# Optimization experiments

Measured on AMD Instinct MI355X. Metric: run time of the kernel, lower is better.

The kernel has to match this reference:

```python
import jax, jax.numpy as jnp
import numpy as np

POOL_SCALES = (1, 3, 6, 8)
CHANNELS = 256
BN_EPS = 1e-5


def _pool_matrix(in_size, out_size):
    # Row i averages input slots [floor(i*in/out), ceil((i+1)*in/out)) -- matches AdaptiveAvgPool2d.
    P = np.zeros((out_size, in_size), np.float32)
    for i in range(out_size):
        s = (i * in_size) // out_size
        e = -((-(i + 1) * in_size) // out_size)
        P[i, s:e] = 1.0 / (e - s)
    return jnp.asarray(P)


def _bn(x, g, b, m, v):
    # inference-mode BatchNorm2d on NCHW
    inv = g * jax.lax.rsqrt(v + BN_EPS)
    return x * inv[None, :, None, None] + (b - m * inv)[None, :, None, None]


def _conv1x1(x, w):
    # 1x1 conv == channel matmul: w [Cout, Cin], x [B, Cin, H, W]
    return jnp.einsum('oc,bchw->bohw', w, x)


def _ppm_concat(x):
    # x: [B, C, H, W] -> [B, C, sum(s*s)]
    B, C, H, W = x.shape
    outs = []
    for s in POOL_SCALES:
        Ph = _pool_matrix(H, s)
        Pw = _pool_matrix(W, s)
        pooled = jnp.einsum('ih,jw,bchw->bcij', Ph, Pw, x)
        outs.append(pooled.reshape(B, C, -1))
    return jnp.concatenate(outs, axis=2)


def setup_inputs() -> dict:
    key = jax.random.key(0)
    ks = jax.random.split(key, 24)
    B, Cl, Ch, Cmid, Cout, H, W = 8, 1024, 2048, 256, 2048, 64, 64
    return {
        'low_feats': jax.random.normal(ks[0], (B, Cl, H, W), jnp.float32),
        'high_feats': jax.random.normal(ks[1], (B, Ch, H, W), jnp.float32),
        'q_w': jax.random.normal(ks[2], (Cmid, Ch), jnp.float32) * 0.02,
        'q_g': jax.random.uniform(ks[3], (Cmid,), jnp.float32, 0.5, 1.5),
        'q_b': jax.random.normal(ks[4], (Cmid,), jnp.float32) * 0.1,
        'q_m': jax.random.normal(ks[5], (Cmid,), jnp.float32) * 0.1,
        'q_v': jax.random.uniform(ks[6], (Cmid,), jnp.float32, 0.5, 1.5),
        'k_w': jax.random.normal(ks[7], (Cmid, Cl), jnp.float32) * 0.02,
        'k_g': jax.random.uniform(ks[8], (Cmid,), jnp.float32, 0.5, 1.5),
        'k_b': jax.random.normal(ks[9], (Cmid,), jnp.float32) * 0.1,
        'k_m': jax.random.normal(ks[10], (Cmid,), jnp.float32) * 0.1,
        'k_v': jax.random.uniform(ks[11], (Cmid,), jnp.float32, 0.5, 1.5),
        'v_w': jax.random.normal(ks[12], (Cmid, Cl), jnp.float32) * 0.02,
        'v_b': jax.random.normal(ks[13], (Cmid,), jnp.float32) * 0.02,
        'o_w': jax.random.normal(ks[14], (Cout, Cmid), jnp.float32) * 0.02,
        'o_b': jax.random.normal(ks[15], (Cout,), jnp.float32) * 0.02,
        'bn_w': jax.random.normal(ks[16], (Cout, Cout + Ch), jnp.float32) * 0.02,
        'bn_g': jax.random.uniform(ks[17], (Cout,), jnp.float32, 0.5, 1.5),
        'bn_b': jax.random.normal(ks[18], (Cout,), jnp.float32) * 0.1,
        'bn_m': jax.random.normal(ks[19], (Cout,), jnp.float32) * 0.1,
        'bn_v': jax.random.uniform(ks[20], (Cout,), jnp.float32, 0.5, 1.5),
    }


def reference(low_feats, high_feats, q_w, q_g, q_b, q_m, q_v,
              k_w, k_g, k_b, k_m, k_v, v_w, v_b, o_w, o_b,
              bn_w, bn_g, bn_b, bn_m, bn_v):
    B, _, H, W = high_feats.shape
    # query: ConvModule (1x1 conv, BN, ReLU) on high-level feats; query_scale=1 -> no downsample
    q = jax.nn.relu(_bn(_conv1x1(high_feats, q_w), q_g, q_b, q_m, q_v))
    q = q.reshape(B, CHANNELS, H * W).transpose(0, 2, 1)  # [B, N, C]
    # key: ConvModule then pyramid-pooled; value: plain 1x1 conv then pyramid-pooled
    k = jax.nn.relu(_bn(_conv1x1(low_feats, k_w), k_g, k_b, k_m, k_v))
    k = _ppm_concat(k)  # [B, C, M]
    v = _conv1x1(low_feats, v_w) + v_b[None, :, None, None]
    v = _ppm_concat(v).transpose(0, 2, 1)  # [B, M, C]
    # matmul-normalized attention with pooled K/V (M = 110, tiny)
    sim = jnp.einsum('bnc,bcm->bnm', q, k) * (CHANNELS ** -0.5)
    sim = jax.nn.softmax(sim, axis=-1)
    ctx = jnp.einsum('bnm,bmc->bnc', sim, v)  # [B, N, C]
    ctx = ctx.transpose(0, 2, 1).reshape(B, CHANNELS, H, W)
    # out projection: plain 1x1 conv with bias
    ctx = _conv1x1(ctx, o_w) + o_b[None, :, None, None]  # [B, Cout, H, W]
    # single stage (query_scales=(1,)), stack+sum is identity
    # bottleneck: 1x1 conv (no bias) + BN, no activation
    fused = jnp.concatenate([ctx, high_feats], axis=1)
    out = _bn(_conv1x1(fused, bn_w), bn_g, bn_b, bn_m, bn_v)
    return out
```

## Files before the change

### kernel.cpp

```cpp
#include <hip/hip_runtime.h>
#include <hip/hip_bf16.h>

typedef unsigned int u32;
typedef unsigned short u16;
typedef short s16x8 __attribute__((ext_vector_type(8)));
typedef float f32x4 __attribute__((ext_vector_type(4)));
typedef u16 u16x4 __attribute__((ext_vector_type(4)));

__device__ __forceinline__ u16 f2b(float x) {
  u32 u = __float_as_uint(x);
  return (u16)((u + 0x7fffu + ((u >> 16) & 1u)) >> 16);
}
__device__ __forceinline__ float b2f(u16 x) { return __uint_as_float(((u32)x) << 16); }

__device__ __forceinline__ void gload16(const void* g, void* l) {
  __builtin_amdgcn_global_load_lds((const __attribute__((address_space(1))) u32*)g,
                                   (__attribute__((address_space(3))) u32*)l, 16, 0, 0);
}
__device__ __forceinline__ f32x4 mfma16(s16x8 a, s16x8 b, f32x4 c) {
  return __builtin_amdgcn_mfma_f32_16x16x32_bf16(a, b, c, 0, 0, 0);
}

template <int OUT_BF16>
__global__ __launch_bounds__(512, 2) void gemm256(
    const u16* __restrict__ A, long long sA, int lda,
    const u16* __restrict__ B1, long long sB1, int K1,
    const u16* __restrict__ B2, long long sB2, int K2,
    void* __restrict__ Cv, long long sC, int ldc,
    const float* __restrict__ bias, int bias_mode,
    int relu_limit, float alpha) {
  const int K = K1 + K2, nt = K >> 6;
  int tm, tn, b;
  {
    const int flat = blockIdx.x + gridDim.x * (blockIdx.y + gridDim.y * blockIdx.z);
    if (gridDim.z == 8) {
      const int slot = flat >> 3;
      b = flat & 7;
      tm = slot % gridDim.x;
      tn = slot / gridDim.x;
    } else { tm = blockIdx.x; tn = blockIdx.y; b = blockIdx.z; }
  }
  const u16* Ab = A + (size_t)b * sA + (size_t)tm * 256 * lda;
  const u16* B1b = B1 + (size_t)b * sB1 + (size_t)tn * 256 * K1;
  const u16* B2b = B2 ? (B2 + (size_t)b * sB2 + (size_t)tn * 256 * K2) : (const u16*)0;

  __shared__ __attribute__((aligned(128))) char lds[131072];

  const int tt = threadIdx.x, w = tt >> 6, l = tt & 63;
  const int wr = w >> 2, wc = w & 3;
  const int lr = l & 15, g16 = l >> 4;
  const int sxl = (lr & 7) << 4;

  auto stage = [&](int kt) {
    const int bufB = (kt & 1) << 16;
    const int kk = kt << 6;
#pragma unroll
    for (int g = 0; g < 4; ++g) {
      const int lin = (g << 13) | (tt << 4);
      const int x = lin ^ (((lin >> 7) & 7) << 4);
      gload16(Ab + (size_t)(x >> 7) * lda + kk + ((x & 127) >> 1),
              lds + bufB + (g << 13) + (w << 10));
    }
    const u16* Bb; int ld, kloc;
    if (kk < K1) { Bb = B1b; ld = K1; kloc = kk; }
    else         { Bb = B2b; ld = K2; kloc = kk - K1; }
#pragma unroll
    for (int g = 0; g < 4; ++g) {
      const int lin = (g << 13) | (tt << 4);
      const int x = lin ^ (((lin >> 7) & 7) << 4);
      gload16(Bb + (size_t)(x >> 7) * ld + kloc + ((x & 127) >> 1),
              lds + bufB + 32768 + (g << 13) + (w << 10));
    }
  };

  stage(0);
  if (nt > 1) stage(1);

  f32x4 acc[8][4] = {};
  s16x8 af[8], bf[4];

  for (int t = 0; t < nt; ++t) {
    const int bufB = (t & 1) << 16;
    const char* Al = lds + bufB;
    const char* Bl = lds + bufB + 32768;
    if (t + 1 < nt) asm volatile("s_waitcnt vmcnt(8)" ::: "memory");
    else            asm volatile("s_waitcnt vmcnt(0)" ::: "memory");
    __builtin_amdgcn_s_barrier();

#pragma unroll
    for (int m = 0; m < 8; ++m)
      af[m] = *reinterpret_cast<const s16x8*>(
          Al + ((wr * 128 + m * 16 + lr) << 7) + ((g16 << 4) ^ sxl));
#pragma unroll
    for (int n = 0; n < 2; ++n)
      bf[n] = *reinterpret_cast<const s16x8*>(
          Bl + ((wc * 64 + n * 16 + lr) << 7) + ((g16 << 4) ^ sxl));
    __builtin_amdgcn_s_barrier();
    asm volatile("s_waitcnt lgkmcnt(0)" ::: "memory");
    __builtin_amdgcn_sched_barrier(0);
    __builtin_amdgcn_s_setprio(1);
#pragma unroll
    for (int m = 0; m < 8; ++m) {
      acc[m][0] = mfma16(af[m], bf[0], acc[m][0]);
      acc[m][1] = mfma16(af[m], bf[1], acc[m][1]);
    }
    __builtin_amdgcn_s_setprio(0);
    __builtin_amdgcn_s_barrier();

#pragma unroll
    for (int n = 2; n < 4; ++n)
      bf[n] = *reinterpret_cast<const s16x8*>(
          Bl + ((wc * 64 + n * 16 + lr) << 7) + ((g16 << 4) ^ sxl));
    __builtin_amdgcn_s_barrier();
    asm volatile("s_waitcnt lgkmcnt(0)" ::: "memory");
    __builtin_amdgcn_sched_barrier(0);
    __builtin_amdgcn_s_setprio(1);
#pragma unroll
    for (int m = 0; m < 8; ++m) {
      acc[m][2] = mfma16(af[m], bf[2], acc[m][2]);
      acc[m][3] = mfma16(af[m], bf[3], acc[m][3]);
    }
    __builtin_amdgcn_s_setprio(0);
    __builtin_amdgcn_s_barrier();

#pragma unroll
    for (int m = 0; m < 8; ++m)
      af[m] = *reinterpret_cast<const s16x8*>(
          Al + ((wr * 128 + m * 16 + lr) << 7) + ((64 | (g16 << 4)) ^ sxl));
#pragma unroll
    for (int n = 0; n < 4; ++n)
      bf[n] = *reinterpret_cast<const s16x8*>(
          Bl + ((wc * 64 + n * 16 + lr) << 7) + ((64 | (g16 << 4)) ^ sxl));
    __builtin_amdgcn_s_barrier();
    asm volatile("s_waitcnt lgkmcnt(0)" ::: "memory");
    __builtin_amdgcn_sched_barrier(0);
    __builtin_amdgcn_s_setprio(1);
#pragma unroll
    for (int m = 0; m < 8; ++m) {
      acc[m][0] = mfma16(af[m], bf[0], acc[m][0]);
      acc[m][1] = mfma16(af[m], bf[1], acc[m][1]);
    }
    __builtin_amdgcn_s_setprio(0);
    __builtin_amdgcn_s_barrier();

    if (t + 2 < nt) stage(t + 2);
    __builtin_amdgcn_s_barrier();
    __builtin_amdgcn_s_setprio(1);
#pragma unroll
    for (int m = 0; m < 8; ++m) {
      acc[m][2] = mfma16(af[m], bf[2], acc[m][2]);
      acc[m][3] = mfma16(af[m], bf[3], acc[m][3]);
    }
    __builtin_amdgcn_s_setprio(0);
    __builtin_amdgcn_s_barrier();
  }

  const int li = g16 * 4;
#pragma unroll
  for (int m = 0; m < 8; ++m) {
    const int row = tm * 256 + wr * 128 + m * 16 + li;
#pragma unroll
    for (int j = 0; j < 4; ++j) {
      const int col = tn * 256 + wc * 64 + j * 16 + lr;
      const float bc = (bias_mode == 1) ? bias[col] : 0.f;
#pragma unroll
      for (int i = 0; i < 4; ++i) {
        float v = acc[m][j][i] * alpha;
        v += (bias_mode == 2) ? bias[row + i] : bc;
        if (col < relu_limit) v = fmaxf(v, 0.f);
        const size_t idx = (size_t)b * sC + (size_t)(row + i) * ldc + col;
        if (OUT_BF16) ((u16*)Cv)[idx] = f2b(v);
        else          ((float*)Cv)[idx] = v;
      }
    }
  }
}

template <int OUT_BF16>
__global__ __launch_bounds__(256) void gemm_bt(
    const u16* __restrict__ A, long long sA, int lda,
    const u16* __restrict__ B1, long long sB1, int K1,
    const u16* __restrict__ B2, long long sB2, int K2,
    void* __restrict__ Cv, long long sC, int ldc,
    const float* __restrict__ bias, int bias_mode,
    int relu_limit, float alpha) {
  const int K = K1 + K2;
  const int b = blockIdx.z;
  const int tm = blockIdx.x, tn = blockIdx.y;
  const u16* Ab = A + (size_t)b * sA;
  const u16* B1b = B1 + (size_t)b * sB1;
  const u16* B2b = B2 ? (B2 + (size_t)b * sB2) : (const u16*)0;

  __shared__ u16 As[128 * 32];
  __shared__ u16 Bs[128 * 32];

  const int t = threadIdx.x;
  const int w = t >> 6, l = t & 63;
  const int wr = w >> 1, wc = w & 1;
  const int srow = w * 16 + (l >> 2);
  const int scol = (l & 3) * 8;
  u16* AsW = As + w * 512;
  u16* BsW = Bs + w * 512;

  f32x4 acc[4][4] = {};
  const int lr = l & 15, lk = (l >> 4) * 8;

  for (int kk = 0; kk < K; kk += 32) {
    __syncthreads();
    {
      const u16* g0 = Ab + (size_t)(tm * 128 + srow) * lda + (kk + scol);
      gload16(g0, AsW);
      gload16(g0 + (size_t)64 * lda, AsW + 2048);
    }
    {
      const u16* bb; int ld, kloc;
      if (kk < K1) { bb = B1b; ld = K1; kloc = kk; }
      else         { bb = B2b; ld = K2; kloc = kk - K1; }
      const u16* g0 = bb + (size_t)(tn * 128 + srow) * ld + (kloc + scol);
      gload16(g0, BsW);
      gload16(g0 + (size_t)64 * ld, BsW + 2048);
    }
    __syncthreads();
    s16x8 af[4], bfr[4];
#pragma unroll
    for (int m = 0; m < 4; ++m)
      af[m] = *reinterpret_cast<const s16x8*>(&As[(wr * 64 + m * 16 + lr) * 32 + lk]);
#pragma unroll
    for (int j = 0; j < 4; ++j)
      bfr[j] = *reinterpret_cast<const s16x8*>(&Bs[(wc * 64 + j * 16 + lr) * 32 + lk]);
#pragma unroll
    for (int m = 0; m < 4; ++m)
#pragma unroll
      for (int j = 0; j < 4; ++j)
        acc[m][j] = mfma16(af[m], bfr[j], acc[m][j]);
  }

  const int li = (l >> 4) * 4;
#pragma unroll
  for (int m = 0; m < 4; ++m) {
    const int row = tm * 128 + wr * 64 + m * 16 + li;
#pragma unroll
    for (int j = 0; j < 4; ++j) {
      const int col = tn * 128 + wc * 64 + j * 16 + lr;
      const float bc = (bias_mode == 1) ? bias[col] : 0.f;
#pragma unroll
      for (int i = 0; i < 4; ++i) {
        float v = acc[m][j][i] * alpha;
        v += (bias_mode == 2) ? bias[row + i] : bc;
        if (col < relu_limit) v = fmaxf(v, 0.f);
        const size_t idx = (size_t)b * sC + (size_t)(row + i) * ldc + col;
        if (OUT_BF16) ((u16*)Cv)[idx] = f2b(v);
        else          ((float*)Cv)[idx] = v;
      }
    }
  }
}

__global__ __launch_bounds__(256) void transpose_cvt(
    const float* __restrict__ in, u16* __restrict__ out, int R, int C) {
  const int b = blockIdx.z;
  in += (size_t)b * R * C;
  out += (size_t)b * R * C;
  const int ct = blockIdx.x, rt = blockIdx.y;
  __shared__ float tile[64][65];
  const int t = threadIdx.x;
  {
    const int c4 = (t & 15) * 4, r0 = t >> 4;
    const float* src = in + (size_t)(rt * 64 + r0) * C + ct * 64 + c4;
#pragma unroll
    for (int i = 0; i < 4; ++i) {
      const float4 v = *reinterpret_cast<const float4*>(src + (size_t)(i * 16) * C);
      tile[r0 + i * 16][c4 + 0] = v.x; tile[r0 + i * 16][c4 + 1] = v.y;
      tile[r0 + i * 16][c4 + 2] = v.z; tile[r0 + i * 16][c4 + 3] = v.w;
    }
  }
  __syncthreads();
  {
    const int r4 = (t & 15) * 4, c0 = t >> 4;
    u16* dst = out + (size_t)(ct * 64 + c0) * R + rt * 64 + r4;
#pragma unroll
    for (int i = 0; i < 4; ++i) {
      u16x4 o;
      o.x = f2b(tile[r4 + 0][c0 + i * 16]);
      o.y = f2b(tile[r4 + 1][c0 + i * 16]);
      o.z = f2b(tile[r4 + 2][c0 + i * 16]);
      o.w = f2b(tile[r4 + 3][c0 + i * 16]);
      *reinterpret_cast<u16x4*>(dst + (size_t)(i * 16) * R) = o;
    }
  }
}

__global__ __launch_bounds__(256) void prep_wq(const float* __restrict__ qw,
    const float* __restrict__ qg, const float* __restrict__ qb_,
    const float* __restrict__ qm, const float* __restrict__ qv,
    u16* __restrict__ Wq, float* __restrict__ qbias) {
  const int i = blockIdx.x * 256 + threadIdx.x;
  const int o = i >> 11, c = i & 2047;
  const float inv = qg[o] * rsqrtf(qv[o] + 1e-5f);
  Wq[i] = f2b(qw[i] * inv);
  if (c == 0) qbias[o] = qb_[o] - qm[o] * inv;
}

__global__ __launch_bounds__(256) void prep_wkv(const float* __restrict__ kw,
    const float* __restrict__ kg, const float* __restrict__ kb,
    const float* __restrict__ km, const float* __restrict__ kv,
    const float* __restrict__ vw, const float* __restrict__ vb,
    u16* __restrict__ Wkv, float* __restrict__ kvbias) {
  const int i = blockIdx.x * 256 + threadIdx.x;
  const int r = i >> 10, c = i & 1023;
  if (r < 256) {
    const float inv = kg[r] * rsqrtf(kv[r] + 1e-5f);
    Wkv[i] = f2b(kw[i] * inv);
    if (c == 0) kvbias[r] = kb[r] - km[r] * inv;
  } else {
    Wkv[i] = f2b(vw[(size_t)(r - 256) * 1024 + c]);
    if (c == 0) kvbias[r] = vb[r - 256];
  }
}

__global__ __launch_bounds__(256) void prep_bn(const float* __restrict__ bn_w,
    const float* __restrict__ g, const float* __restrict__ v_,
    u16* __restrict__ bn1s, u16* __restrict__ Wfin) {
  const int i = blockIdx.x * 256 + threadIdx.x;
  const int o = i >> 11, j = i & 2047;
  const float inv = g[o] * rsqrtf(v_[o] + 1e-5f);
  bn1s[i] = f2b(bn_w[(size_t)o * 4096 + j] * inv);
  Wfin[(size_t)o * 2304 + j] = f2b(bn_w[(size_t)o * 4096 + 2048 + j] * inv);
}

__global__ __launch_bounds__(256) void prep_fbias(const float* __restrict__ bn_w,
    const float* __restrict__ o_b, const float* __restrict__ g,
    const float* __restrict__ bb, const float* __restrict__ m_,
    const float* __restrict__ v_, float* __restrict__ fbias) {
  const int o = blockIdx.x, t = threadIdx.x;
  float s = 0.f;
  for (int j = t; j < 2048; j += 256) s += bn_w[(size_t)o * 4096 + j] * o_b[j];
  for (int off = 32; off; off >>= 1) s += __shfl_xor(s, off);
  __shared__ float red[4];
  if ((t & 63) == 0) red[t >> 6] = s;
  __syncthreads();
  if (t == 0) {
    const float tot = red[0] + red[1] + red[2] + red[3];
    const float inv = g[o] * rsqrtf(v_[o] + 1e-5f);
    fbias[o] = inv * tot + bb[o] - m_[o] * inv;
  }
}

__device__ __forceinline__ void jj_to_range(int jj, int& s, int& j, int& c0, int& c1) {
  if (jj < 1)       { s = 1; j = jj; }
  else if (jj < 4)  { s = 3; j = jj - 1; }
  else if (jj < 10) { s = 6; j = jj - 4; }
  else              { s = 8; j = jj - 10; }
  c0 = (j * 64) / s;
  c1 = ((j + 1) * 64 + s - 1) / s;
}

__global__ __launch_bounds__(256) void pool_cols(const u16* __restrict__ kvT,
                                                 float* __restrict__ cp) {
  const int b = blockIdx.y, r = blockIdx.x, t = threadIdx.x;
  const u16* base = kvT + ((size_t)b * 4096 + (size_t)r * 64) * 512;
  const int ch0 = (t & 63) * 8;
  for (int jj = (t >> 6); jj < 18; jj += 4) {
    int s, j, c0, c1;
    jj_to_range(jj, s, j, c0, c1);
    float acc[8] = {0.f, 0.f, 0.f, 0.f, 0.f, 0.f, 0.f, 0.f};
    for (int c = c0; c < c1; ++c) {
      const s16x8 v = *reinterpret_cast<const s16x8*>(base + (size_t)c * 512 + ch0);
#pragma unroll
      for (int i = 0; i < 8; ++i) acc[i] += b2f((u16)v[i]);
    }
    float* o = cp + (((size_t)(b * 64 + r) * 18 + jj) * 512 + ch0);
    *reinterpret_cast<float4*>(o)     = make_float4(acc[0], acc[1], acc[2], acc[3]);
    *reinterpret_cast<float4*>(o + 4) = make_float4(acc[4], acc[5], acc[6], acc[7]);
  }
}

__global__ __launch_bounds__(256) void pool_rows(const float* __restrict__ cp,
    u16* __restrict__ Kp, u16* __restrict__ Vp) {
  const int b = blockIdx.y, m = blockIdx.x, t = threadIdx.x;
  if (m >= 110) {
    Kp[((size_t)b * 128 + m) * 256 + t] = 0;
    Vp[((size_t)b * 256 + t) * 128 + m] = 0;
    return;
  }
  int s, idx, jjbase;
  if (m < 1)       { s = 1; idx = m;      jjbase = 0; }
  else if (m < 10) { s = 3; idx = m - 1;  jjbase = 1; }
  else if (m < 46) { s = 6; idx = m - 10; jjbase = 4; }
  else             { s = 8; idx = m - 46; jjbase = 10; }
  const int i = idx / s, j = idx % s;
  const int jj = jjbase + j;
  const int r0 = (i * 64) / s, r1 = ((i + 1) * 64 + s - 1) / s;
  const int c0 = (j * 64) / s, c1 = ((j + 1) * 64 + s - 1) / s;
  float a0 = 0.f, a1 = 0.f;
  for (int r = r0; r < r1; ++r) {
    const float* px = cp + ((size_t)(b * 64 + r) * 18 + jj) * 512;
    a0 += px[t];
    a1 += px[t + 256];
  }
  const float inv = 1.f / (float)((r1 - r0) * (c1 - c0));
  Kp[((size_t)b * 128 + m) * 256 + t] = f2b(a0 * inv);
  Vp[((size_t)b * 256 + t) * 128 + m] = f2b(a1 * inv);
}

__global__ __launch_bounds__(256) void softmax_rows(const float* __restrict__ sim,
                                                    u16* __restrict__ P) {
  const int row = blockIdx.x * 4 + (threadIdx.x >> 6);
  const int l = threadIdx.x & 63;
  const float* s = sim + (size_t)row * 128;
  const float v0 = (l < 110) ? s[l] : -1e30f;
  const float v1 = (l + 64 < 110) ? s[l + 64] : -1e30f;
  float mx = fmaxf(v0, v1);
  for (int off = 32; off; off >>= 1) mx = fmaxf(mx, __shfl_xor(mx, off));
  const float e0 = (l < 110) ? __expf(v0 - mx) : 0.f;
  const float e1 = (l + 64 < 110) ? __expf(v1 - mx) : 0.f;
  float sum = e0 + e1;
  for (int off = 32; off; off >>= 1) sum += __shfl_xor(sum, off);
  const float inv = 1.f / sum;
  u16* p = P + (size_t)row * 128;
  p[l] = f2b(e0 * inv);
  p[l + 64] = f2b(e1 * inv);
}

extern "C" void kernel_launch(void* const* d_in, const int* in_sizes, int n_in,
                              void* d_out, int out_size, void* d_ws, size_t ws_size,
                              hipStream_t stream) {
  (void)in_sizes; (void)n_in; (void)out_size; (void)ws_size;
  const float* low  = (const float*)d_in[0];
  const float* high = (const float*)d_in[1];
  const float* q_w = (const float*)d_in[2];
  const float* q_g = (const float*)d_in[3];
  const float* q_b = (const float*)d_in[4];
  const float* q_m = (const float*)d_in[5];
  const float* q_v = (const float*)d_in[6];
  const float* k_w = (const float*)d_in[7];
  const float* k_g = (const float*)d_in[8];
  const float* k_b = (const float*)d_in[9];
  const float* k_m = (const float*)d_in[10];
  const float* k_v = (const float*)d_in[11];
  const float* v_w = (const float*)d_in[12];
  const float* v_b = (const float*)d_in[13];
  const float* o_w = (const float*)d_in[14];
  const float* o_b = (const float*)d_in[15];
  const float* bn_w = (const float*)d_in[16];
  const float* bn_g = (const float*)d_in[17];
  const float* bn_b = (const float*)d_in[18];
  const float* bn_m = (const float*)d_in[19];
  const float* bn_v = (const float*)d_in[20];
  float* out = (float*)d_out;

  char* ws = (char*)d_ws;
  size_t off = 0;
  auto alloc = [&](size_t bytes) -> char* {
    char* p = ws + off;
    off += (bytes + 255) & ~(size_t)255;
    return p;
  };
  u16* XhT  = (u16*)alloc(134217728ull);
  u16* qT   = (u16*)alloc(16777216ull);
  u16* XlT  = (u16*)alloc(67108864ull);
  u16* kvT  = (u16*)alloc(33554432ull);
  u16* ctxT = (u16*)alloc(16777216ull);
  u16* Kpool = (u16*)alloc(524288ull);
  u16* VpT   = (u16*)alloc(524288ull);
  u16* Wq   = (u16*)alloc(1048576ull);
  u16* Wkv  = (u16*)alloc(1048576ull);
  u16* Wfin = (u16*)alloc(9437184ull);
  float* qbias  = (float*)alloc(1024);
  float* kvbias = (float*)alloc(2048);
  float* fbias  = (float*)alloc(8192);
  u16* bn1s = qT;
  u16* owT  = ctxT;
  float* sim = (float*)XlT;
  float* cp  = (float*)((char*)XlT + 25165824ull);
  u16* P = kvT;

  prep_bn<<<16384, 256, 0, stream>>>(bn_w, bn_g, bn_v, bn1s, Wfin);
  prep_fbias<<<2048, 256, 0, stream>>>(bn_w, o_b, bn_g, bn_b, bn_m, bn_v, fbias);
  prep_wq<<<2048, 256, 0, stream>>>(q_w, q_g, q_b, q_m, q_v, Wq, qbias);
  prep_wkv<<<2048, 256, 0, stream>>>(k_w, k_g, k_b, k_m, k_v, v_w, v_b, Wkv, kvbias);
  transpose_cvt<<<dim3(4, 32, 1), 256, 0, stream>>>(o_w, owT, 2048, 256);
  gemm_bt<1><<<dim3(16, 2, 1), 256, 0, stream>>>(
      bn1s, 0, 2048, owT, 0, 2048, (const u16*)0, 0, 0,
      (void*)(Wfin + 2048), 0, 2304, (const float*)0, 0, 0, 1.0f);

  transpose_cvt<<<dim3(64, 32, 8), 256, 0, stream>>>(high, XhT, 2048, 4096);
  transpose_cvt<<<dim3(64, 16, 8), 256, 0, stream>>>(low, XlT, 1024, 4096);

  gemm_bt<1><<<dim3(32, 2, 8), 256, 0, stream>>>(
      XhT, 4096ll * 2048, 2048, Wq, 0, 2048, (const u16*)0, 0, 0,
      qT, 4096ll * 256, 256, qbias, 1, 256, 1.0f);
  gemm256<1><<<dim3(16, 2, 8), 512, 0, stream>>>(
      XlT, 4096ll * 1024, 1024, Wkv, 0, 1024, (const u16*)0, 0, 0,
      kvT, 4096ll * 512, 512, kvbias, 1, 256, 1.0f);
  pool_cols<<<dim3(64, 8), 256, 0, stream>>>(kvT, cp);
  pool_rows<<<dim3(128, 8), 256, 0, stream>>>(cp, Kpool, VpT);
  gemm_bt<0><<<dim3(32, 1, 8), 256, 0, stream>>>(
      qT, 4096ll * 256, 256, Kpool, 128ll * 256, 256, (const u16*)0, 0, 0,
      sim, 4096ll * 128, 128, (const float*)0, 0, 0, 0.0625f);
  softmax_rows<<<8192, 256, 0, stream>>>(sim, P);
  gemm_bt<1><<<dim3(32, 2, 8), 256, 0, stream>>>(
      P, 4096ll * 128, 128, VpT, 256ll * 128, 128, (const u16*)0, 0, 0,
      ctxT, 4096ll * 256, 256, (const float*)0, 0, 0, 1.0f);
  gemm256<0><<<dim3(8, 16, 8), 512, 0, stream>>>(
      Wfin, 0, 2304, XhT, 4096ll * 2048, 2048, ctxT, 4096ll * 256, 256,
      out, 2048ll * 4096, 4096, fbias, 2, 0, 1.0f);
}
```

Measured before the change: 796.7 us.

## Split GEMM tile staging into quarter loads interleaved across MFMA phases

Restructures the main GEMM k-loop so global-to-LDS loads for A are issued in row quarters and for B in halves, spread across the four MFMA phases of each iteration instead of issued as one batch. Fragment loads now cover half of the M rows per phase with separate B fragment buffers for each k-half, which lowers live A fragment registers. The aim is smoother overlap of memory traffic with MFMA work and less register pressure, at the cost of more intricate vmcnt accounting, where a wrong count could read incomplete LDS data.

```diff
diff --git a/kernel.cpp b/kernel.cpp
--- a/kernel.cpp
+++ b/kernel.cpp
@@ -51,107 +51,108 @@
   const int lr = l & 15, g16 = l >> 4;
   const int sxl = (lr & 7) << 4;
 
-  auto stage = [&](int kt) {
+  auto stage_Aq = [&](int kt, int q) {
     const int bufB = (kt & 1) << 16;
     const int kk = kt << 6;
-#pragma unroll
-    for (int g = 0; g < 4; ++g) {
+    const int lin = tt << 4;
+    const int x = lin ^ (((lin >> 7) & 7) << 4);
+    gload16(Ab + (size_t)((q << 6) + (x >> 7)) * lda + kk + ((x & 127) >> 1),
+            lds + bufB + (q << 13) + (w << 10));
+  };
+  auto stage_Bh = [&](int kt, int h) {
+    const int bufB = (kt & 1) << 16;
+    const int kk = kt << 6;
+    const u16* src; int ld, kcol;
+    if (kk < K1) { src = B1b; ld = K1; kcol = kk; }
+    else         { src = B2b; ld = K2; kcol = kk - K1; }
+#pragma unroll
+    for (int g = 0; g < 2; ++g) {
       const int lin = (g << 13) | (tt << 4);
       const int x = lin ^ (((lin >> 7) & 7) << 4);
-      gload16(Ab + (size_t)(x >> 7) * lda + kk + ((x & 127) >> 1),
-              lds + bufB + (g << 13) + (w << 10));
-    }
-    const u16* Bb; int ld, kloc;
-    if (kk < K1) { Bb = B1b; ld = K1; kloc = kk; }
-    else         { Bb = B2b; ld = K2; kloc = kk - K1; }
-#pragma unroll
-    for (int g = 0; g < 4; ++g) {
-      const int lin = (g << 13) | (tt << 4);
-      const int x = lin ^ (((lin >> 7) & 7) << 4);
-      gload16(Bb + (size_t)(x >> 7) * ld + kloc + ((x & 127) >> 1),
-              lds + bufB + 32768 + (g << 13) + (w << 10));
+      gload16(src + (size_t)((h << 7) + (x >> 7)) * ld + kcol + ((x & 127) >> 1),
+              lds + bufB + 32768 + (h << 14) + (g << 13) + (w << 10));
     }
   };
 
-  stage(0);
-  if (nt > 1) stage(1);
+  auto lda_frag = [&](const char* Al, int h, int kk, s16x8* af) {
+#pragma unroll
+    for (int i = 0; i < 4; ++i) {
+      const int row = wr * 128 + (h * 4 + i) * 16 + lr;
+      af[i] = *reinterpret_cast<const s16x8*>(
+          Al + (row << 7) + (((kk << 6) | (g16 << 4)) ^ sxl));
+    }
+  };
+  auto ldb_frag = [&](const char* Bl, int kk, s16x8* bf) {
+#pragma unroll
+    for (int n = 0; n < 4; ++n) {
+      const int row = wc * 64 + n * 16 + lr;
+      bf[n] = *reinterpret_cast<const s16x8*>(
+          Bl + (row << 7) + (((kk << 6) | (g16 << 4)) ^ sxl));
+    }
+  };
 
   f32x4 acc[8][4] = {};
-  s16x8 af[8], bf[4];
+
+  auto mfma_q = [&](int h, const s16x8* af, const s16x8* bf) {
+    __builtin_amdgcn_s_setprio(1);
+#pragma unroll
+    for (int i = 0; i < 4; ++i)
+#pragma unroll
+      for (int n = 0; n < 4; ++n)
+        acc[h * 4 + i][n] = mfma16(af[i], bf[n], acc[h * 4 + i][n]);
+    __builtin_amdgcn_s_setprio(0);
+  };
+
+  stage_Aq(0, 0); stage_Aq(0, 2); stage_Bh(0, 0); stage_Bh(0, 1);
+  stage_Aq(0, 1); stage_Aq(0, 3);
+  if (nt > 1) {
+    stage_Aq(1, 0); stage_Aq(1, 2); stage_Bh(1, 0); stage_Bh(1, 1);
+    asm volatile("s_waitcnt vmcnt(6)" ::: "memory");
+  } else {
+    asm volatile("s_waitcnt vmcnt(0)" ::: "memory");
+  }
+  __builtin_amdgcn_s_barrier();
 
   for (int t = 0; t < nt; ++t) {
-    const int bufB = (t & 1) << 16;
-    const char* Al = lds + bufB;
-    const char* Bl = lds + bufB + 32768;
-    if (t + 1 < nt) asm volatile("s_waitcnt vmcnt(8)" ::: "memory");
-    else            asm volatile("s_waitcnt vmcnt(0)" ::: "memory");
-    __builtin_amdgcn_s_barrier();
-
-#pragma unroll
-    for (int m = 0; m < 8; ++m)
-      af[m] = *reinterpret_cast<const s16x8*>(
-          Al + ((wr * 128 + m * 16 + lr) << 7) + ((g16 << 4) ^ sxl));
-#pragma unroll
-    for (int n = 0; n < 2; ++n)
-      bf[n] = *reinterpret_cast<const s16x8*>(
-          Bl + ((wc * 64 + n * 16 + lr) << 7) + ((g16 << 4) ^ sxl));
+    const char* Al = lds + ((t & 1) << 16);
+    const char* Bl = Al + 32768;
+    s16x8 bf0[4], bf1[4], af[4];
+
+    lda_frag(Al, 0, 0, af);
+    ldb_frag(Bl, 0, bf0);
+    if (t + 1 < nt) { stage_Aq(t + 1, 1); stage_Aq(t + 1, 3); }
     __builtin_amdgcn_s_barrier();
     asm volatile("s_waitcnt lgkmcnt(0)" ::: "memory");
     __builtin_amdgcn_sched_barrier(0);
-    __builtin_amdgcn_s_setprio(1);
-#pragma unroll
-    for (int m = 0; m < 8; ++m) {
-      acc[m][0] = mfma16(af[m], bf[0], acc[m][0]);
-      acc[m][1] = mfma16(af[m], bf[1], acc[m][1]);
-    }
-    __builtin_amdgcn_s_setprio(0);
-    __builtin_amdgcn_s_barrier();
-
-#pragma unroll
-    for (int n = 2; n < 4; ++n)
-      bf[n] = *reinterpret_cast<const s16x8*>(
-          Bl + ((wc * 64 + n * 16 + lr) << 7) + ((g16 << 4) ^ sxl));
+    mfma_q(0, af, bf0);
+    __builtin_amdgcn_s_barrier();
+
+    lda_frag(Al, 0, 1, af);
+    ldb_frag(Bl, 1, bf1);
     __builtin_amdgcn_s_barrier();
     asm volatile("s_waitcnt lgkmcnt(0)" ::: "memory");
     __builtin_amdgcn_sched_barrier(0);
-    __builtin_amdgcn_s_setprio(1);
-#pragma unroll
-    for (int m = 0; m < 8; ++m) {
-      acc[m][2] = mfma16(af[m], bf[2], acc[m][2]);
-      acc[m][3] = mfma16(af[m], bf[3], acc[m][3]);
-    }
-    __builtin_amdgcn_s_setprio(0);
-    __builtin_amdgcn_s_barrier();
-
-#pragma unroll
-    for (int m = 0; m < 8; ++m)
-      af[m] = *reinterpret_cast<const s16x8*>(
-          Al + ((wr * 128 + m * 16 + lr) << 7) + ((64 | (g16 << 4)) ^ sxl));
-#pragma unroll
-    for (int n = 0; n < 4; ++n)
-      bf[n] = *reinterpret_cast<const s16x8*>(
-          Bl + ((wc * 64 + n * 16 + lr) << 7) + ((64 | (g16 << 4)) ^ sxl));
+    mfma_q(0, af, bf1);
+    __builtin_amdgcn_s_barrier();
+
+    lda_frag(Al, 1, 0, af);
+    if (t + 2 < nt) { stage_Aq(t + 2, 0); stage_Aq(t + 2, 2); stage_Bh(t + 2, 0); }
     __builtin_amdgcn_s_barrier();
     asm volatile("s_waitcnt lgkmcnt(0)" ::: "memory");
     __builtin_amdgcn_sched_barrier(0);
-    __builtin_amdgcn_s_setprio(1);
-#pragma unroll
-    for (int m = 0; m < 8; ++m) {
-      acc[m][0] = mfma16(af[m], bf[0], acc[m][0]);
-      acc[m][1] = mfma16(af[m], bf[1], acc[m][1]);
-    }
-    __builtin_amdgcn_s_setprio(0);
-    __builtin_amdgcn_s_barrier();
-
-    if (t + 2 < nt) stage(t + 2);
-    __builtin_amdgcn_s_barrier();
-    __builtin_amdgcn_s_setprio(1);
-#pragma unroll
-    for (int m = 0; m < 8; ++m) {
-      acc[m][2] = mfma16(af[m], bf[2], acc[m][2]);
-      acc[m][3] = mfma16(af[m], bf[3], acc[m][3]);
-    }
-    __builtin_amdgcn_s_setprio(0);
+    mfma_q(1, af, bf0);
+    __builtin_amdgcn_s_barrier();
+
+    lda_frag(Al, 1, 1, af);
+    if (t + 2 < nt) stage_Bh(t + 2, 1);
+    __builtin_amdgcn_s_barrier();
+    asm volatile("s_waitcnt lgkmcnt(0)" ::: "memory");
+    __builtin_amdgcn_sched_barrier(0);
+    mfma_q(1, af, bf1);
+    if (t + 1 < nt) {
+      if (t + 2 < nt) asm volatile("s_waitcnt vmcnt(6)" ::: "memory");
+      else            asm volatile("s_waitcnt vmcnt(0)" ::: "memory");
+    }
     __builtin_amdgcn_s_barrier();
   }
 
```

After: 766.6 us. 3.8% less time.
